# Optimization experiments

Hardware: AMD Instinct MI355X
Metric: run time of the kernel (lower is better)

Reference implementation:

```python
import jax, jax.numpy as jnp
import numpy as np

EPS = 1e-5
VPL_LAMBDA = 0.15
START_ITERS = 8000
ALLOWED_DELTA = 200


def _l2norm(v, axis):
    # F.normalize(v, p=2, dim=axis, eps=1e-5): v / max(||v||, eps)
    n = jnp.sqrt(jnp.sum(v * v, axis=axis, keepdims=True))
    return v / jnp.maximum(n, EPS)


def setup_inputs() -> dict:
    key = jax.random.key(0)
    k1, k2, k3, k4 = jax.random.split(key, 4)
    B, I, O = 512, 4096, 4096  # code requires in_features == out_features
    x = jax.random.normal(k1, (B, I), jnp.float32)
    xavier_std = (2.0 / (I + O)) ** 0.5
    weight = jax.random.normal(k2, (O, I), jnp.float32) * xavier_std
    queue_features = jax.random.normal(k3, (O, I), jnp.float32)
    # mix of active (delta<=200) and stale entries so torch.where path is exercised
    queue_iters = jax.random.randint(k4, (O,), 9700, 10100, dtype=jnp.int32)
    iters = jnp.asarray(10000, jnp.int32)  # > start_iters -> VPL blend active
    return {"x": x, "weight": weight, "queue_features": queue_features,
            "queue_iters": queue_iters, "iters": iters}


def reference(x, weight, queue_features, queue_iters, iters):
    it = iters + 1  # forward does self.iters += 1 before comparisons
    active = (it - queue_iters) <= ALLOWED_DELTA  # [O]
    ql = jnp.where((it > START_ITERS) & active, VPL_LAMBDA, 0.0).astype(x.dtype)  # [O]
    norm_inputs = _l2norm(x, 1)            # [B, I]
    norm_w = _l2norm(weight, 0)            # [O, I], column-wise L2 norm (dim=0)
    ql_e = ql[:, None]                     # [O, 1]
    # queue_features.t() is [I, O]; broadcast add valid because O == I
    injected = norm_w * (1.0 - ql_e) + queue_features.T * ql_e  # [O, I]
    injected = _l2norm(injected, 0)        # renormalize columns
    # F.linear(norm_inputs, injected.t()) == norm_inputs @ injected
    return norm_inputs @ injected          # [B, O]
```

## Files before the change

### kernel.cpp

```cpp
#include <hip/hip_runtime.h>
#include <hip/hip_bf16.h>
#include <stdint.h>

#define EPS 1e-5f
#define LAMBDA 0.15f
#define START_ITERS 8000
#define ALLOWED_DELTA 200

typedef __attribute__((ext_vector_type(4))) float f32x4;
typedef __attribute__((ext_vector_type(8))) short bf16x8;

__device__ __forceinline__ ushort f2bf(float f) {
  union { float f; uint32_t u; } v = {f};
  uint32_t u = v.u;
  return (ushort)((u + 0x7FFF + ((u >> 16) & 1)) >> 16);
}
__device__ __forceinline__ float bf2f(ushort b) {
  union { uint32_t u; float f; } v; v.u = ((uint32_t)b) << 16; return v.f;
}

__device__ __forceinline__ void gload16(const void* g, void* l) {
  __builtin_amdgcn_global_load_lds(
      (const __attribute__((address_space(1))) void*)(uintptr_t)(g),
      (__attribute__((address_space(3))) void*)(uint32_t)(uintptr_t)(l),
      16, 0, 0);
}

__global__ __launch_bounds__(256) void k_rownorm(const float* __restrict__ x,
                                                 ushort* __restrict__ nx) {
  const int K = 4096;
  int r = blockIdx.x, t = threadIdx.x;
  const f32x4* xr = (const f32x4*)(x + (size_t)r * K);
  f32x4 v[4];
  float s = 0.f;
#pragma unroll
  for (int p = 0; p < 4; ++p) {
    v[p] = xr[p * 256 + t];
    s += v[p].x * v[p].x + v[p].y * v[p].y + v[p].z * v[p].z + v[p].w * v[p].w;
  }
#pragma unroll
  for (int m = 1; m < 64; m <<= 1) s += __shfl_xor(s, m);
  __shared__ float red[4];
  if ((t & 63) == 0) red[t >> 6] = s;
  __syncthreads();
  float inv = 1.f / fmaxf(sqrtf(red[0] + red[1] + red[2] + red[3]), EPS);
#pragma unroll
  for (int p = 0; p < 4; ++p) {
    ushort4 o;
    o.x = f2bf(v[p].x * inv); o.y = f2bf(v[p].y * inv);
    o.z = f2bf(v[p].z * inv); o.w = f2bf(v[p].w * inv);
    *(ushort4*)(nx + (size_t)r * K + (size_t)(p * 256 + t) * 4) = o;
  }
}

__global__ __launch_bounds__(256) void k_wsumsq(const float* __restrict__ w,
                                                float* __restrict__ wsumsq) {
  const int N = 4096;
  int t = threadIdx.x;
  int c = blockIdx.x * 1024 + t * 4;
  int a0 = blockIdx.y * 64;
  f32x4 acc = {0.f, 0.f, 0.f, 0.f};
  for (int a = a0; a < a0 + 64; ++a) {
    f32x4 v = *(const f32x4*)(w + (size_t)a * N + c);
    acc += v * v;
  }
  atomicAdd(&wsumsq[c + 0], acc.x);
  atomicAdd(&wsumsq[c + 1], acc.y);
  atomicAdd(&wsumsq[c + 2], acc.z);
  atomicAdd(&wsumsq[c + 3], acc.w);
}

__global__ __launch_bounds__(256) void k_prep(const int* __restrict__ qiters,
                                              const int* __restrict__ iters,
                                              const float* __restrict__ wsumsq,
                                              float* __restrict__ ql,
                                              float* __restrict__ winv) {
  int i = blockIdx.x * 256 + threadIdx.x;
  int it = iters[0] + 1;
  bool act = (it - qiters[i]) <= ALLOWED_DELTA;
  ql[i] = (it > START_ITERS && act) ? LAMBDA : 0.f;
  winv[i] = 1.f / fmaxf(sqrtf(wsumsq[i]), EPS);
}

__global__ __launch_bounds__(256) void k_combine(const float* __restrict__ w,
                                                 const float* __restrict__ qf,
                                                 const float* __restrict__ ql,
                                                 const float* __restrict__ winv,
                                                 ushort* __restrict__ injT,
                                                 float* __restrict__ injss) {
  const int N = 4096;
  __shared__ float wt[64][65];
  __shared__ float qls[64];
  __shared__ float wis[64];
  int a0 = blockIdx.y * 64, c0 = blockIdx.x * 64;
  int t = threadIdx.x;
  if (t < 64) qls[t] = ql[a0 + t];
  else if (t < 128) wis[t - 64] = winv[c0 + (t - 64)];
  int rr = t >> 4, cc = (t & 15) * 4;
#pragma unroll
  for (int p = 0; p < 4; ++p) {
    int ar = p * 16 + rr;
    f32x4 v = *(const f32x4*)(w + (size_t)(a0 + ar) * N + c0 + cc);
    wt[ar][cc + 0] = v.x; wt[ar][cc + 1] = v.y;
    wt[ar][cc + 2] = v.z; wt[ar][cc + 3] = v.w;
  }
  __syncthreads();
  int al = (t & 15) * 4;
#pragma unroll
  for (int p = 0; p < 4; ++p) {
    int c = p * 16 + rr;
    f32x4 q4 = *(const f32x4*)(qf + (size_t)(c0 + c) * N + a0 + al);
    float wi = wis[c];
    float ss = 0.f;
    ushort4 ob;
#pragma unroll
    for (int j = 0; j < 4; ++j) {
      float qla = qls[al + j];
      float val = wt[al + j][c] * wi * (1.f - qla) + q4[j] * qla;
      ushort b = f2bf(val);
      float vb = bf2f(b);
      ss += vb * vb;
      ((ushort*)&ob)[j] = b;
    }
    *(ushort4*)(injT + (size_t)(c0 + c) * N + a0 + al) = ob;
    ss += __shfl_xor(ss, 1); ss += __shfl_xor(ss, 2);
    ss += __shfl_xor(ss, 4); ss += __shfl_xor(ss, 8);
    if ((t & 15) == 0) atomicAdd(&injss[c0 + c], ss);
  }
}

__global__ __launch_bounds__(256) void k_scale(const float* __restrict__ injss,
                                               float* __restrict__ scale) {
  int i = blockIdx.x * 256 + threadIdx.x;
  scale[i] = 1.f / fmaxf(sqrtf(injss[i]), EPS);
}

__global__ __launch_bounds__(256) void k_gemm(const ushort* __restrict__ A,
                                              const ushort* __restrict__ B,
                                              const float* __restrict__ scale,
                                              float* __restrict__ C) {
  const int N = 4096, K = 4096, BK = 64;
  __shared__ __align__(16) ushort As[2][8][64][8];
  __shared__ __align__(16) ushort Bs[2][8][64][8];
  int tile_m = blockIdx.y * 64, tile_n = blockIdx.x * 64;
  int t = threadIdx.x;
  int lane = t & 63, wid = t >> 6;
  int wm = wid >> 1, wn = wid & 1;
  int q = lane >> 4, fr = lane & 15;

  const ushort* aSrc = A + (size_t)(tile_m + lane) * K + wid * 16;
  const ushort* bSrc = B + (size_t)(tile_n + lane) * K + wid * 16;

  f32x4 acc[2][2] = {};

  auto stage = [&](int buf, int k0) {
    gload16(aSrc + k0,     &As[buf][2 * wid][0][0]);
    gload16(aSrc + k0 + 8, &As[buf][2 * wid + 1][0][0]);
    gload16(bSrc + k0,     &Bs[buf][2 * wid][0][0]);
    gload16(bSrc + k0 + 8, &Bs[buf][2 * wid + 1][0][0]);
  };

  stage(0, 0);
  __syncthreads();
  const int NT = K / BK;
  for (int kt = 0; kt < NT; ++kt) {
    int cur = kt & 1;
    if (kt + 1 < NT) stage(cur ^ 1, (kt + 1) * BK);
#pragma unroll
    for (int kk = 0; kk < 2; ++kk) {
      int kbi = kk * 4 + q;
      bf16x8 af[2], bfv[2];
#pragma unroll
      for (int m = 0; m < 2; ++m)
        af[m] = *(const bf16x8*)&As[cur][kbi][wm * 32 + m * 16 + fr][0];
#pragma unroll
      for (int n = 0; n < 2; ++n)
        bfv[n] = *(const bf16x8*)&Bs[cur][kbi][wn * 32 + n * 16 + fr][0];
#pragma unroll
      for (int m = 0; m < 2; ++m)
#pragma unroll
        for (int n = 0; n < 2; ++n)
          acc[m][n] = __builtin_amdgcn_mfma_f32_16x16x32_bf16(af[m], bfv[n], acc[m][n], 0, 0, 0);
    }
    __syncthreads();
  }
#pragma unroll
  for (int m = 0; m < 2; ++m) {
    int row0 = tile_m + wm * 32 + m * 16 + q * 4;
#pragma unroll
    for (int n = 0; n < 2; ++n) {
      int col = tile_n + wn * 32 + n * 16 + fr;
      float sc = scale[col];
#pragma unroll
      for (int r = 0; r < 4; ++r)
        C[(size_t)(row0 + r) * N + col] = acc[m][n][r] * sc;
    }
  }
}

extern "C" void kernel_launch(void* const* d_in, const int* in_sizes, int n_in,
                              void* d_out, int out_size, void* d_ws, size_t ws_size,
                              hipStream_t stream) {
  const float* x   = (const float*)d_in[0];
  const float* w   = (const float*)d_in[1];
  const float* qf  = (const float*)d_in[2];
  const int*   qit = (const int*)d_in[3];
  const int*   its = (const int*)d_in[4];
  float* out = (float*)d_out;

  char* ws = (char*)d_ws;
  ushort* nx   = (ushort*)ws;
  ushort* injT = (ushort*)(ws + (4u << 20));
  float* stats = (float*)(ws + (36u << 20));
  float* wsumsq = stats;
  float* injss  = stats + 4096;
  float* ql     = stats + 8192;
  float* winv   = stats + 12288;
  float* scale  = stats + 16384;

  hipMemsetAsync(stats, 0, 2 * 4096 * sizeof(float), stream);
  k_rownorm<<<512, 256, 0, stream>>>(x, nx);
  k_wsumsq<<<dim3(4, 64), 256, 0, stream>>>(w, wsumsq);
  k_prep<<<16, 256, 0, stream>>>(qit, its, wsumsq, ql, winv);
  k_combine<<<dim3(64, 64), 256, 0, stream>>>(w, qf, ql, winv, injT, injss);
  k_scale<<<16, 256, 0, stream>>>(injss, scale);
  k_gemm<<<dim3(64, 8), 256, 0, stream>>>(nx, injT, scale, out);
}
```

Before: 249.1 us.

## Triple-buffer GEMM k-loop and fold prep/scale kernels into consumers

Result: faster. 242.7 us (-2.6%).

```diff
diff --git a/kernel.cpp b/kernel.cpp
--- a/kernel.cpp
+++ b/kernel.cpp
@@ -70,22 +70,11 @@
   atomicAdd(&wsumsq[c + 3], acc.w);
 }
 
-__global__ __launch_bounds__(256) void k_prep(const int* __restrict__ qiters,
-                                              const int* __restrict__ iters,
-                                              const float* __restrict__ wsumsq,
-                                              float* __restrict__ ql,
-                                              float* __restrict__ winv) {
-  int i = blockIdx.x * 256 + threadIdx.x;
-  int it = iters[0] + 1;
-  bool act = (it - qiters[i]) <= ALLOWED_DELTA;
-  ql[i] = (it > START_ITERS && act) ? LAMBDA : 0.f;
-  winv[i] = 1.f / fmaxf(sqrtf(wsumsq[i]), EPS);
-}
-
 __global__ __launch_bounds__(256) void k_combine(const float* __restrict__ w,
                                                  const float* __restrict__ qf,
-                                                 const float* __restrict__ ql,
-                                                 const float* __restrict__ winv,
+                                                 const int* __restrict__ qiters,
+                                                 const int* __restrict__ iters,
+                                                 const float* __restrict__ wsumsq,
                                                  ushort* __restrict__ injT,
                                                  float* __restrict__ injss) {
   const int N = 4096;
@@ -94,8 +83,13 @@
   __shared__ float wis[64];
   int a0 = blockIdx.y * 64, c0 = blockIdx.x * 64;
   int t = threadIdx.x;
-  if (t < 64) qls[t] = ql[a0 + t];
-  else if (t < 128) wis[t - 64] = winv[c0 + (t - 64)];
+  if (t < 64) {
+    int it = iters[0] + 1;
+    bool act = (it - qiters[a0 + t]) <= ALLOWED_DELTA;
+    qls[t] = (it > START_ITERS && act) ? LAMBDA : 0.f;
+  } else if (t < 128) {
+    wis[t - 64] = 1.f / fmaxf(sqrtf(wsumsq[c0 + (t - 64)]), EPS);
+  }
   int rr = t >> 4, cc = (t & 15) * 4;
 #pragma unroll
   for (int p = 0; p < 4; ++p) {
@@ -129,19 +123,13 @@
   }
 }
 
-__global__ __launch_bounds__(256) void k_scale(const float* __restrict__ injss,
-                                               float* __restrict__ scale) {
-  int i = blockIdx.x * 256 + threadIdx.x;
-  scale[i] = 1.f / fmaxf(sqrtf(injss[i]), EPS);
-}
-
 __global__ __launch_bounds__(256) void k_gemm(const ushort* __restrict__ A,
                                               const ushort* __restrict__ B,
-                                              const float* __restrict__ scale,
+                                              const float* __restrict__ injss,
                                               float* __restrict__ C) {
   const int N = 4096, K = 4096, BK = 64;
-  __shared__ __align__(16) ushort As[2][8][64][8];
-  __shared__ __align__(16) ushort Bs[2][8][64][8];
+  __shared__ __align__(16) ushort As[3][8][64][8];
+  __shared__ __align__(16) ushort Bs[3][8][64][8];
   int tile_m = blockIdx.y * 64, tile_n = blockIdx.x * 64;
   int t = threadIdx.x;
   int lane = t & 63, wid = t >> 6;
@@ -153,44 +141,55 @@
 
   f32x4 acc[2][2] = {};
 
-  auto stage = [&](int buf, int k0) {
+  auto stage = [&](int buf, int kt) {
+    int k0 = kt * BK;
     gload16(aSrc + k0,     &As[buf][2 * wid][0][0]);
     gload16(aSrc + k0 + 8, &As[buf][2 * wid + 1][0][0]);
     gload16(bSrc + k0,     &Bs[buf][2 * wid][0][0]);
     gload16(bSrc + k0 + 8, &Bs[buf][2 * wid + 1][0][0]);
   };
-
-  stage(0, 0);
-  __syncthreads();
-  const int NT = K / BK;
-  for (int kt = 0; kt < NT; ++kt) {
-    int cur = kt & 1;
-    if (kt + 1 < NT) stage(cur ^ 1, (kt + 1) * BK);
+  auto compute = [&](int buf) {
 #pragma unroll
     for (int kk = 0; kk < 2; ++kk) {
       int kbi = kk * 4 + q;
       bf16x8 af[2], bfv[2];
 #pragma unroll
       for (int m = 0; m < 2; ++m)
-        af[m] = *(const bf16x8*)&As[cur][kbi][wm * 32 + m * 16 + fr][0];
+        af[m] = *(const bf16x8*)&As[buf][kbi][wm * 32 + m * 16 + fr][0];
 #pragma unroll
       for (int n = 0; n < 2; ++n)
-        bfv[n] = *(const bf16x8*)&Bs[cur][kbi][wn * 32 + n * 16 + fr][0];
+        bfv[n] = *(const bf16x8*)&Bs[buf][kbi][wn * 32 + n * 16 + fr][0];
 #pragma unroll
       for (int m = 0; m < 2; ++m)
 #pragma unroll
         for (int n = 0; n < 2; ++n)
           acc[m][n] = __builtin_amdgcn_mfma_f32_16x16x32_bf16(af[m], bfv[n], acc[m][n], 0, 0, 0);
     }
-    __syncthreads();
-  }
+  };
+
+  const int NT = K / BK;
+  stage(0, 0);
+  stage(1, 1);
+  asm volatile("s_waitcnt vmcnt(4)" ::: "memory");
+  __builtin_amdgcn_s_barrier();
+  for (int kt = 0; kt < NT - 2; ++kt) {
+    stage((kt + 2) % 3, kt + 2);
+    compute(kt % 3);
+    asm volatile("s_waitcnt vmcnt(4)" ::: "memory");
+    __builtin_amdgcn_s_barrier();
+  }
+  compute((NT - 2) % 3);
+  asm volatile("s_waitcnt vmcnt(0)" ::: "memory");
+  __builtin_amdgcn_s_barrier();
+  compute((NT - 1) % 3);
+
 #pragma unroll
   for (int m = 0; m < 2; ++m) {
     int row0 = tile_m + wm * 32 + m * 16 + q * 4;
 #pragma unroll
     for (int n = 0; n < 2; ++n) {
       int col = tile_n + wn * 32 + n * 16 + fr;
-      float sc = scale[col];
+      float sc = 1.f / fmaxf(sqrtf(injss[col]), EPS);
 #pragma unroll
       for (int r = 0; r < 4; ++r)
         C[(size_t)(row0 + r) * N + col] = acc[m][n][r] * sc;
@@ -214,15 +213,10 @@
   float* stats = (float*)(ws + (36u << 20));
   float* wsumsq = stats;
   float* injss  = stats + 4096;
-  float* ql     = stats + 8192;
-  float* winv   = stats + 12288;
-  float* scale  = stats + 16384;
 
   hipMemsetAsync(stats, 0, 2 * 4096 * sizeof(float), stream);
   k_rownorm<<<512, 256, 0, stream>>>(x, nx);
   k_wsumsq<<<dim3(4, 64), 256, 0, stream>>>(w, wsumsq);
-  k_prep<<<16, 256, 0, stream>>>(qit, its, wsumsq, ql, winv);
-  k_combine<<<dim3(64, 64), 256, 0, stream>>>(w, qf, ql, winv, injT, injss);
-  k_scale<<<16, 256, 0, stream>>>(injss, scale);
-  k_gemm<<<dim3(64, 8), 256, 0, stream>>>(nx, injT, scale, out);
-}
+  k_combine<<<dim3(64, 64), 256, 0, stream>>>(w, qf, qit, its, wsumsq, injT, injss);
+  k_gemm<<<dim3(64, 8), 256, 0, stream>>>(nx, injT, injss, out);
+}
```
